# Kernel tuning notes

Hardware: AMD Instinct MI355X
Metric: run time of the kernel (lower is better)

The kernel has to match this reference:

```python
import jax, jax.numpy as jnp
import numpy as np

N, E, G = 100000, 800000, 1
DV, DE, DU, H = 64, 32, 32, 128

def _w(key, shape):
    return jax.random.normal(key, shape, dtype=jnp.float32) * 0.05

def setup_inputs() -> dict:
    key = jax.random.key(0)
    ks = jax.random.split(key, 16)
    inp = {
        "node_attr": jax.random.normal(ks[0], (N, DV), dtype=jnp.float32),
        "edges": jax.random.randint(ks[1], (2, E), 0, N, dtype=jnp.int64 if jax.config.jax_enable_x64 else jnp.int32),
        "edge_attr": jax.random.normal(ks[2], (E, DE), dtype=jnp.float32),
        "u": jax.random.normal(ks[3], (G, DU), dtype=jnp.float32),
        "node_idx": jnp.zeros((N,), dtype=jnp.int32),
        "edge_idx": jnp.zeros((E,), dtype=jnp.int32),
        # edge MLP: concat(src, dst, edge_attr, u) -> H -> H
        "W1e": _w(ks[4], (2 * DV + DE + DU, H)), "b1e": jnp.zeros((H,), jnp.float32),
        "W2e": _w(ks[5], (H, H)), "b2e": jnp.zeros((H,), jnp.float32),
        # node MLP: concat(node_attr, aggregated_edges, u) -> H -> H
        "W1n": _w(ks[6], (DV + H + DU, H)), "b1n": jnp.zeros((H,), jnp.float32),
        "W2n": _w(ks[7], (H, H)), "b2n": jnp.zeros((H,), jnp.float32),
        # global MLP: concat(node_mean, edge_mean, u) -> H -> H
        "W1g": _w(ks[8], (H + H + DU, H)), "b1g": jnp.zeros((H,), jnp.float32),
        "W2g": _w(ks[9], (H, H)), "b2g": jnp.zeros((H,), jnp.float32),
    }
    return inp

def _mlp(x, W1, b1, W2, b2):
    return jax.nn.relu(x @ W1 + b1) @ W2 + b2

def _seg_mean(x, seg, num):
    s = jax.ops.segment_sum(x, seg, num_segments=num)
    c = jax.ops.segment_sum(jnp.ones((x.shape[0], 1), x.dtype), seg, num_segments=num)
    return s / jnp.maximum(c, 1.0)

def reference(node_attr, edges, edge_attr, u, node_idx, edge_idx,
              W1e, b1e, W2e, b2e, W1n, b1n, W2n, b2n, W1g, b1g, W2g, b2g):
    row, col = edges[0], edges[1]
    # edge model: gather endpoint features, concat with edge/global attrs
    e_in = jnp.concatenate([node_attr[row], node_attr[col], edge_attr, u[edge_idx]], axis=-1)
    e = _mlp(e_in, W1e, b1e, W2e, b2e)                        # [E, H]
    # node model: scatter-add incoming edge messages onto receivers (col)
    agg = jax.ops.segment_sum(e, col, num_segments=node_attr.shape[0])  # [N, H]
    v_in = jnp.concatenate([node_attr, agg, u[node_idx]], axis=-1)
    v = _mlp(v_in, W1n, b1n, W2n, b2n)                        # [N, H]
    # global model: per-graph mean pooling of nodes and edges
    nv = _seg_mean(v, node_idx, u.shape[0])                   # [G, H]
    ne = _seg_mean(e, edge_idx, u.shape[0])                   # [G, H]
    g_in = jnp.concatenate([nv, ne, u], axis=-1)
    g = _mlp(g_in, W1g, b1g, W2g, b2g)                        # [G, H]
    return v, e, g
```

## Files before the change

kernel.cpp:

```cpp
#include <hip/hip_runtime.h>

#define N_NODES 100000
#define N_EDGES 800000
#define DV 64
#define DE 32
#define DU 32
#define H 128

#define NTILES 12500

typedef short bf16x8 __attribute__((ext_vector_type(8)));
typedef unsigned short u16;
typedef u16 u16x8 __attribute__((ext_vector_type(8)));
typedef float f32x4 __attribute__((ext_vector_type(4)));

#define OFF_ESUM 0
#define OFF_VSUM 8192
#define OFF_BIAS 16384
#define OFF_PART 17408
#define OFF_WBUF 19456
#define OFF_DEG  175104
#define OFF_SE   575104
#define OFF_DSTP 6975104

#define W1ET_OFF 0
#define W2ET_OFF 20480
#define W1NT_OFF 36864
#define W2NT_OFF 61440
#define WBUF_ELEMS 77824

#define NPART 391

__device__ inline u16 f2bf(float x) {
  union { float f; unsigned u; } c; c.f = x;
  unsigned r = c.u + 0x7FFFu + ((c.u >> 16) & 1u);
  return (u16)(r >> 16);
}

__global__ void prep_weights(const float* __restrict__ W1e, const float* __restrict__ W2e,
                             const float* __restrict__ W1n, const float* __restrict__ W2n,
                             u16* __restrict__ wbuf) {
  int i = blockIdx.x * blockDim.x + threadIdx.x;
  if (i < 20480) {
    int j = i / 160, k = i - j * 160;
    wbuf[W1ET_OFF + i] = f2bf(W1e[k * H + j]);
  } else if (i < 36864) {
    int t = i - 20480; int j = t >> 7, k = t & 127;
    wbuf[i] = f2bf(W2e[k * H + j]);
  } else if (i < 61440) {
    int t = i - 36864; int j = t / 192, k = t - j * 192;
    wbuf[i] = f2bf(W1n[k * H + j]);
  } else if (i < WBUF_ELEMS) {
    int t = i - 61440; int j = t >> 7, k = t & 127;
    wbuf[i] = f2bf(W2n[k * H + j]);
  }
}

__global__ void prep_bias(const float* __restrict__ uattr,
                          const float* __restrict__ W1e, const float* __restrict__ b1e,
                          const float* __restrict__ W1n, const float* __restrict__ b1n,
                          float* __restrict__ bias) {
  int t = threadIdx.x;
  float be = b1e[t];
  float bn = b1n[t];
  for (int k = 0; k < DU; ++k) {
    float uk = uattr[k];
    be += uk * W1e[(2 * DV + DE + k) * H + t];
    bn += uk * W1n[(DV + H + k) * H + t];
  }
  bias[t] = be;
  bias[128 + t] = bn;
}

__global__ void degree_kernel(const int* __restrict__ edges, int* __restrict__ deg) {
  int i = blockIdx.x * 256 + threadIdx.x;
  if (i < N_EDGES) atomicAdd(&deg[edges[N_EDGES + i]], 1);
}

__global__ void scan_part(const int* __restrict__ deg, int* __restrict__ part) {
  int i = blockIdx.x * 256 + threadIdx.x;
  int v = (i < N_NODES) ? deg[i] : 0;
#pragma unroll
  for (int m = 1; m < 64; m <<= 1) v += __shfl_xor(v, m);
  __shared__ int s[4];
  if ((threadIdx.x & 63) == 0) s[threadIdx.x >> 6] = v;
  __syncthreads();
  if (threadIdx.x == 0) part[blockIdx.x] = s[0] + s[1] + s[2] + s[3];
}

__global__ void scan_top(int* __restrict__ part) {
  __shared__ int s[512];
  int t = threadIdx.x;
  s[t] = (t < NPART) ? part[t] : 0;
  __syncthreads();
  for (int d = 1; d < 512; d <<= 1) {
    int v = (t >= d) ? s[t - d] : 0;
    __syncthreads();
    s[t] += v;
    __syncthreads();
  }
  if (t < NPART) part[t] = (t == 0) ? 0 : s[t - 1];
}

__global__ void scan_down(const int* __restrict__ part, int* __restrict__ deg_cursor) {
  __shared__ int s[256];
  int b = blockIdx.x, t = threadIdx.x;
  int i = b * 256 + t;
  int v = (i < N_NODES) ? deg_cursor[i] : 0;
  s[t] = v;
  __syncthreads();
  for (int d = 1; d < 256; d <<= 1) {
    int u = (t >= d) ? s[t - d] : 0;
    __syncthreads();
    s[t] += u;
    __syncthreads();
  }
  int excl = s[t] - v + part[b];
  if (i < N_NODES) deg_cursor[i] = excl;
}

__global__ void fill_kernel(const int* __restrict__ edges, int* __restrict__ cursor,
                            int2* __restrict__ se, int* __restrict__ dstP) {
  int i = blockIdx.x * 256 + threadIdx.x;
  if (i < N_EDGES) {
    int s = edges[i];
    int d = edges[N_EDGES + i];
    int pos = atomicAdd(&cursor[d], 1);
    se[pos] = make_int2(s, i);
    dstP[pos] = d;
  }
}

__global__ __launch_bounds__(256, 4) void edge_kernel(
    const float* __restrict__ node_attr, const float* __restrict__ edge_attr,
    const u16* __restrict__ wbuf, const float* __restrict__ bias_f,
    const float* __restrict__ b2,
    const int2* __restrict__ se, const int* __restrict__ dstP,
    float* __restrict__ e_out, float* __restrict__ agg, float* __restrict__ esum_p)
{
  __shared__ __align__(16) char smem[37888];
  u16 (*X)[164]    = (u16(*)[164])smem;
  u16 (*Hs)[132]   = (u16(*)[132])(smem + 20992);
  float (*OT)[132] = (float(*)[132])smem;
  __shared__ int sSrc[64], sEid[64], sDst[64];

  const int tid = threadIdx.x;
  const int wave = tid >> 6, lane = tid & 63;
  const int l15 = lane & 15, lg = lane >> 4;
  const int wc = wave * 32;

  int b = blockIdx.x;
  const int q = NTILES / 8, r8 = NTILES % 8;
  int xcd = b & 7, pos = b >> 3;
  long t = (xcd < r8 ? xcd * (q + 1) : r8 * (q + 1) + (xcd - r8) * q) + pos;
  const long i0 = t * 64;

  if (tid < 64)        { int2 v = se[i0 + tid]; sSrc[tid] = v.x; sEid[tid] = v.y; }
  else if (tid < 128)  sDst[tid - 64] = dstP[i0 + (tid - 64)];

  bf16x8 w1[5][2];
  {
    const u16* w1t = wbuf + W1ET_OFF;
#pragma unroll
    for (int cf = 0; cf < 2; ++cf) {
      const u16* p1 = w1t + (wc + cf * 16 + l15) * 160 + lg * 8;
#pragma unroll
      for (int ks = 0; ks < 5; ++ks) w1[ks][cf] = *(const bf16x8*)(p1 + ks * 32);
    }
  }
  float bias1[2] = { bias_f[wc + l15], bias_f[wc + 16 + l15] };

  __syncthreads();

#pragma unroll
  for (int it = 0; it < 5; ++it) {
    int ch = tid + it * 256;
    int r = ch / 20, g = ch - r * 20;
    int col = g * 8;
    const float* src;
    if (col < 64)        src = node_attr + (long)sSrc[r] * DV + col;
    else if (col < 128)  src = node_attr + (long)sDst[r] * DV + (col - 64);
    else                 src = edge_attr + (long)sEid[r] * DE + (col - 128);
    float4 f0 = *(const float4*)src;
    float4 f1 = *(const float4*)(src + 4);
    u16x8 p;
    p[0] = f2bf(f0.x); p[1] = f2bf(f0.y); p[2] = f2bf(f0.z); p[3] = f2bf(f0.w);
    p[4] = f2bf(f1.x); p[5] = f2bf(f1.y); p[6] = f2bf(f1.z); p[7] = f2bf(f1.w);
    *(u16x8*)&X[r][col] = p;
  }

  __syncthreads();

  f32x4 acc[4][2];
#pragma unroll
  for (int rf = 0; rf < 4; ++rf)
#pragma unroll
    for (int cf = 0; cf < 2; ++cf)
#pragma unroll
      for (int j = 0; j < 4; ++j) acc[rf][cf][j] = 0.f;

#pragma unroll
  for (int ks = 0; ks < 5; ++ks) {
#pragma unroll
    for (int rf = 0; rf < 4; ++rf) {
      bf16x8 a = *(const bf16x8*)&X[rf * 16 + l15][ks * 32 + lg * 8];
      acc[rf][0] = __builtin_amdgcn_mfma_f32_16x16x32_bf16(a, w1[ks][0], acc[rf][0], 0, 0, 0);
      acc[rf][1] = __builtin_amdgcn_mfma_f32_16x16x32_bf16(a, w1[ks][1], acc[rf][1], 0, 0, 0);
    }
  }

  bf16x8 w2[4][2];
  {
    const u16* w2t = wbuf + W2ET_OFF;
#pragma unroll
    for (int cf = 0; cf < 2; ++cf) {
      const u16* p2 = w2t + (wc + cf * 16 + l15) * 128 + lg * 8;
#pragma unroll
      for (int ks = 0; ks < 4; ++ks) w2[ks][cf] = *(const bf16x8*)(p2 + ks * 32);
    }
  }
  float bias2[2] = { b2[wc + l15], b2[wc + 16 + l15] };

#pragma unroll
  for (int rf = 0; rf < 4; ++rf)
#pragma unroll
    for (int cf = 0; cf < 2; ++cf)
#pragma unroll
      for (int j = 0; j < 4; ++j) {
        float hv = acc[rf][cf][j] + bias1[cf];
        hv = hv > 0.f ? hv : 0.f;
        Hs[rf * 16 + lg * 4 + j][wc + cf * 16 + l15] = f2bf(hv);
      }

  __syncthreads();

#pragma unroll
  for (int rf = 0; rf < 4; ++rf)
#pragma unroll
    for (int cf = 0; cf < 2; ++cf)
#pragma unroll
      for (int j = 0; j < 4; ++j) acc[rf][cf][j] = 0.f;

#pragma unroll
  for (int ks = 0; ks < 4; ++ks) {
#pragma unroll
    for (int rf = 0; rf < 4; ++rf) {
      bf16x8 a = *(const bf16x8*)&Hs[rf * 16 + l15][ks * 32 + lg * 8];
      acc[rf][0] = __builtin_amdgcn_mfma_f32_16x16x32_bf16(a, w2[ks][0], acc[rf][0], 0, 0, 0);
      acc[rf][1] = __builtin_amdgcn_mfma_f32_16x16x32_bf16(a, w2[ks][1], acc[rf][1], 0, 0, 0);
    }
  }

  __syncthreads();

  float es0 = 0.f, es1 = 0.f;
#pragma unroll
  for (int rf = 0; rf < 4; ++rf) {
#pragma unroll
    for (int cf = 0; cf < 2; ++cf) {
#pragma unroll
      for (int j = 0; j < 4; ++j) {
        float v = acc[rf][cf][j] + bias2[cf];
        OT[rf * 16 + lg * 4 + j][wc + cf * 16 + l15] = v;
        if (cf == 0) es0 += v; else es1 += v;
      }
    }
  }

  __syncthreads();

#pragma unroll
  for (int i = 0; i < 8; ++i) {
    int ch = tid + i * 256;
    int r = ch >> 5, c4 = ch & 31;
    float4 f = *(const float4*)&OT[r][c4 * 4];
    *(float4*)(e_out + (long)sEid[r] * H + c4 * 4) = f;
  }

  {
    const int c = tid & 127;
    const int rlo = (tid >> 7) * 32;
    float sum = 0.f;
    int runStart = rlo;
#pragma unroll 8
    for (int r = rlo; r < rlo + 32; ++r) {
      sum += OT[r][c];
      bool bnd = (r == rlo + 31) || (sDst[r + 1] != sDst[r]);
      if (bnd) {
        float* p = &agg[(long)sDst[r] * H + c];
        if (runStart == rlo || r == rlo + 31) atomicAdd(p, sum);
        else *p = sum;
        sum = 0.f; runStart = r + 1;
      }
    }
  }

#pragma unroll
  for (int m = 16; m < 64; m <<= 1) { es0 += __shfl_xor(es0, m); es1 += __shfl_xor(es1, m); }
  if (lane < 16) {
    atomicAdd(&esum_p[(wc + lane) * 16], es0);
    atomicAdd(&esum_p[(wc + 16 + lane) * 16], es1);
  }
}

__global__ __launch_bounds__(256, 3) void node_kernel(
    const float* __restrict__ node_attr, const u16* __restrict__ wbuf,
    const float* __restrict__ bias_f, const float* __restrict__ b2,
    float* __restrict__ vio, float* __restrict__ vsum_p)
{
  __shared__ __align__(16) u16 X[64][196];
  __shared__ __align__(16) u16 Hs[64][132];

  const int tid = threadIdx.x;
  const int wave = tid >> 6, lane = tid & 63;
  const int l15 = lane & 15, lg = lane >> 4;
  const long n0 = (long)blockIdx.x * 64;
  const int wc = wave * 32;

#pragma unroll
  for (int it = 0; it < 6; ++it) {
    int ch = tid + it * 256;
    int r = ch / 24, g = ch - r * 24;
    int col = g * 8;
    long n = n0 + r; if (n >= N_NODES) n = N_NODES - 1;
    const float* src;
    if (col < 64)  src = node_attr + n * DV + col;
    else           src = vio + n * H + (col - 64);
    float4 f0 = *(const float4*)src;
    float4 f1 = *(const float4*)(src + 4);
    u16x8 p;
    p[0] = f2bf(f0.x); p[1] = f2bf(f0.y); p[2] = f2bf(f0.z); p[3] = f2bf(f0.w);
    p[4] = f2bf(f1.x); p[5] = f2bf(f1.y); p[6] = f2bf(f1.z); p[7] = f2bf(f1.w);
    *(u16x8*)&X[r][col] = p;
  }

  bf16x8 w1[6][2], w2[4][2];
  {
    const u16* w1t = wbuf + W1NT_OFF;
    const u16* w2t = wbuf + W2NT_OFF;
#pragma unroll
    for (int cf = 0; cf < 2; ++cf) {
      const u16* p1 = w1t + (wc + cf * 16 + l15) * 192 + lg * 8;
#pragma unroll
      for (int ks = 0; ks < 6; ++ks) w1[ks][cf] = *(const bf16x8*)(p1 + ks * 32);
      const u16* p2 = w2t + (wc + cf * 16 + l15) * 128 + lg * 8;
#pragma unroll
      for (int ks = 0; ks < 4; ++ks) w2[ks][cf] = *(const bf16x8*)(p2 + ks * 32);
    }
  }

  __syncthreads();

  f32x4 acc[4][2];
#pragma unroll
  for (int rf = 0; rf < 4; ++rf)
#pragma unroll
    for (int cf = 0; cf < 2; ++cf)
#pragma unroll
      for (int j = 0; j < 4; ++j) acc[rf][cf][j] = 0.f;

#pragma unroll
  for (int ks = 0; ks < 6; ++ks) {
#pragma unroll
    for (int rf = 0; rf < 4; ++rf) {
      bf16x8 a = *(const bf16x8*)&X[rf * 16 + l15][ks * 32 + lg * 8];
      acc[rf][0] = __builtin_amdgcn_mfma_f32_16x16x32_bf16(a, w1[ks][0], acc[rf][0], 0, 0, 0);
      acc[rf][1] = __builtin_amdgcn_mfma_f32_16x16x32_bf16(a, w1[ks][1], acc[rf][1], 0, 0, 0);
    }
  }

  float bias1[2] = { bias_f[128 + wc + l15], bias_f[128 + wc + 16 + l15] };
#pragma unroll
  for (int rf = 0; rf < 4; ++rf)
#pragma unroll
    for (int cf = 0; cf < 2; ++cf)
#pragma unroll
      for (int j = 0; j < 4; ++j) {
        float hv = acc[rf][cf][j] + bias1[cf];
        hv = hv > 0.f ? hv : 0.f;
        Hs[rf * 16 + lg * 4 + j][wc + cf * 16 + l15] = f2bf(hv);
      }

  __syncthreads();

#pragma unroll
  for (int rf = 0; rf < 4; ++rf)
#pragma unroll
    for (int cf = 0; cf < 2; ++cf)
#pragma unroll
      for (int j = 0; j < 4; ++j) acc[rf][cf][j] = 0.f;

#pragma unroll
  for (int ks = 0; ks < 4; ++ks) {
#pragma unroll
    for (int rf = 0; rf < 4; ++rf) {
      bf16x8 a = *(const bf16x8*)&Hs[rf * 16 + l15][ks * 32 + lg * 8];
      acc[rf][0] = __builtin_amdgcn_mfma_f32_16x16x32_bf16(a, w2[ks][0], acc[rf][0], 0, 0, 0);
      acc[rf][1] = __builtin_amdgcn_mfma_f32_16x16x32_bf16(a, w2[ks][1], acc[rf][1], 0, 0, 0);
    }
  }

  float bias2[2] = { b2[wc + l15], b2[wc + 16 + l15] };
  float vs0 = 0.f, vs1 = 0.f;
#pragma unroll
  for (int rf = 0; rf < 4; ++rf) {
#pragma unroll
    for (int cf = 0; cf < 2; ++cf) {
      int colg = wc + cf * 16 + l15;
#pragma unroll
      for (int j = 0; j < 4; ++j) {
        int r = rf * 16 + lg * 4 + j;
        long n = n0 + r;
        if (n < N_NODES) {
          float v = acc[rf][cf][j] + bias2[cf];
          vio[n * H + colg] = v;
          if (cf == 0) vs0 += v; else vs1 += v;
        }
      }
    }
  }
#pragma unroll
  for (int m = 16; m < 64; m <<= 1) { vs0 += __shfl_xor(vs0, m); vs1 += __shfl_xor(vs1, m); }
  if (lane < 16) {
    atomicAdd(&vsum_p[(wc + lane) * 16], vs0);
    atomicAdd(&vsum_p[(wc + 16 + lane) * 16], vs1);
  }
}

__global__ void global_kernel(const float* __restrict__ uattr,
    const float* __restrict__ W1g, const float* __restrict__ b1g,
    const float* __restrict__ W2g, const float* __restrict__ b2g,
    const float* __restrict__ esum_p, const float* __restrict__ vsum_p,
    float* __restrict__ g_out)
{
  __shared__ float gin[288];
  __shared__ float hbuf[128];
  int t = threadIdx.x;
  gin[t]       = vsum_p[t * 16] * (1.f / (float)N_NODES);
  gin[128 + t] = esum_p[t * 16] * (1.f / (float)N_EDGES);
  if (t < 32) gin[256 + t] = uattr[t];
  __syncthreads();
  float a = b1g[t];
  for (int k = 0; k < 288; ++k) a += gin[k] * W1g[k * H + t];
  hbuf[t] = fmaxf(a, 0.f);
  __syncthreads();
  float b = b2g[t];
  for (int k = 0; k < 128; ++k) b += hbuf[k] * W2g[k * H + t];
  g_out[t] = b;
}

extern "C" void kernel_launch(void* const* d_in, const int* in_sizes, int n_in,
                              void* d_out, int out_size, void* d_ws, size_t ws_size,
                              hipStream_t stream) {
  const float* node_attr = (const float*)d_in[0];
  const int*   edges     = (const int*)d_in[1];
  const float* edge_attr = (const float*)d_in[2];
  const float* uattr     = (const float*)d_in[3];
  const float* W1e = (const float*)d_in[6];  const float* b1e = (const float*)d_in[7];
  const float* W2e = (const float*)d_in[8];  const float* b2e = (const float*)d_in[9];
  const float* W1n = (const float*)d_in[10]; const float* b1n = (const float*)d_in[11];
  const float* W2n = (const float*)d_in[12]; const float* b2n = (const float*)d_in[13];
  const float* W1g = (const float*)d_in[14]; const float* b1g = (const float*)d_in[15];
  const float* W2g = (const float*)d_in[16]; const float* b2g = (const float*)d_in[17];

  float* out   = (float*)d_out;
  float* v_out = out;
  float* e_out = out + (long)N_NODES * H;
  float* g_out = out + (long)N_NODES * H + (long)N_EDGES * H;

  char* ws = (char*)d_ws;
  float* esum_p = (float*)(ws + OFF_ESUM);
  float* vsum_p = (float*)(ws + OFF_VSUM);
  float* bias_f = (float*)(ws + OFF_BIAS);
  int*   part   = (int*)(ws + OFF_PART);
  u16*   wbuf   = (u16*)(ws + OFF_WBUF);
  int*   deg    = (int*)(ws + OFF_DEG);
  int2*  se     = (int2*)(ws + OFF_SE);
  int*   dstP   = (int*)(ws + OFF_DSTP);

  hipMemsetAsync(ws, 0, 16384, stream);
  hipMemsetAsync(deg, 0, N_NODES * sizeof(int), stream);
  hipMemsetAsync(v_out, 0, (size_t)N_NODES * H * sizeof(float), stream);

  prep_weights<<<WBUF_ELEMS / 256, 256, 0, stream>>>(W1e, W2e, W1n, W2n, wbuf);
  prep_bias<<<1, 128, 0, stream>>>(uattr, W1e, b1e, W1n, b1n, bias_f);
  degree_kernel<<<(N_EDGES + 255) / 256, 256, 0, stream>>>(edges, deg);
  scan_part<<<NPART, 256, 0, stream>>>(deg, part);
  scan_top<<<1, 512, 0, stream>>>(part);
  scan_down<<<NPART, 256, 0, stream>>>(part, deg);
  fill_kernel<<<(N_EDGES + 255) / 256, 256, 0, stream>>>(edges, deg, se, dstP);

  edge_kernel<<<NTILES, 256, 0, stream>>>(node_attr, edge_attr, wbuf,
                                          bias_f, b2e, se, dstP,
                                          e_out, v_out, esum_p);
  node_kernel<<<(N_NODES + 63) / 64, 256, 0, stream>>>(node_attr, wbuf,
                                                       bias_f, b2n, v_out, vsum_p);
  global_kernel<<<1, 128, 0, stream>>>(uattr, W1g, b1g, W2g, b2g, esum_p, vsum_p, g_out);
}
```

Baseline: 665.3 us.

## Replace atomic scatter aggregation with CSR gather in node kernel

The edge kernel now processes edges in their original order, so the edge_attr reads and e_out writes are contiguous, and it no longer scatters messages into agg with atomics. The node kernel instead walks a CSR bucket of incoming edge ids and sums their e_out rows to build the aggregate, which also removes the v_out memset. Both kernels move to 512-thread blocks with larger tiles. The cost is an extra random read of e_out (800K×128 floats) in the node kernel, and the row-run coalescing of atomics that the sorted layout gave is lost.

```diff
diff --git a/kernel.cpp b/kernel.cpp
--- a/kernel.cpp
+++ b/kernel.cpp
@@ -7,7 +7,8 @@
 #define DU 32
 #define H 128
 
-#define NTILES 12500
+#define ETILE 128
+#define NTILES_E (N_EDGES / ETILE)
 
 typedef short bf16x8 __attribute__((ext_vector_type(8)));
 typedef unsigned short u16;
@@ -20,8 +21,8 @@
 #define OFF_PART 17408
 #define OFF_WBUF 19456
 #define OFF_DEG  175104
-#define OFF_SE   575104
-#define OFF_DSTP 6975104
+#define OFF_OFFS 575104
+#define OFF_BUCK 975104
 
 #define W1ET_OFF 0
 #define W2ET_OFF 20480
@@ -102,7 +103,8 @@
   if (t < NPART) part[t] = (t == 0) ? 0 : s[t - 1];
 }
 
-__global__ void scan_down(const int* __restrict__ part, int* __restrict__ deg_cursor) {
+__global__ void scan_down(const int* __restrict__ part, int* __restrict__ deg_cursor,
+                          int* __restrict__ offsets) {
   __shared__ int s[256];
   int b = blockIdx.x, t = threadIdx.x;
   int i = b * 256 + t;
@@ -116,47 +118,41 @@
     __syncthreads();
   }
   int excl = s[t] - v + part[b];
-  if (i < N_NODES) deg_cursor[i] = excl;
+  if (i < N_NODES) { offsets[i] = excl; deg_cursor[i] = excl; }
 }
 
 __global__ void fill_kernel(const int* __restrict__ edges, int* __restrict__ cursor,
-                            int2* __restrict__ se, int* __restrict__ dstP) {
+                            int* __restrict__ bucket) {
   int i = blockIdx.x * 256 + threadIdx.x;
   if (i < N_EDGES) {
-    int s = edges[i];
     int d = edges[N_EDGES + i];
     int pos = atomicAdd(&cursor[d], 1);
-    se[pos] = make_int2(s, i);
-    dstP[pos] = d;
-  }
-}
-
-__global__ __launch_bounds__(256, 4) void edge_kernel(
-    const float* __restrict__ node_attr, const float* __restrict__ edge_attr,
+    bucket[pos] = i;
+  }
+}
+
+__global__ __launch_bounds__(512, 2) void edge_kernel(
+    const float* __restrict__ node_attr, const int* __restrict__ edges,
+    const float* __restrict__ edge_attr,
     const u16* __restrict__ wbuf, const float* __restrict__ bias_f,
     const float* __restrict__ b2,
-    const int2* __restrict__ se, const int* __restrict__ dstP,
-    float* __restrict__ e_out, float* __restrict__ agg, float* __restrict__ esum_p)
+    float* __restrict__ e_out, float* __restrict__ esum_p)
 {
-  __shared__ __align__(16) char smem[37888];
+  __shared__ __align__(16) char smem[75776];
   u16 (*X)[164]    = (u16(*)[164])smem;
-  u16 (*Hs)[132]   = (u16(*)[132])(smem + 20992);
+  u16 (*Hs)[132]   = (u16(*)[132])(smem + 41984);
   float (*OT)[132] = (float(*)[132])smem;
-  __shared__ int sSrc[64], sEid[64], sDst[64];
+  __shared__ int sSrc[128], sDst[128];
 
   const int tid = threadIdx.x;
   const int wave = tid >> 6, lane = tid & 63;
   const int l15 = lane & 15, lg = lane >> 4;
-  const int wc = wave * 32;
-
-  int b = blockIdx.x;
-  const int q = NTILES / 8, r8 = NTILES % 8;
-  int xcd = b & 7, pos = b >> 3;
-  long t = (xcd < r8 ? xcd * (q + 1) : r8 * (q + 1) + (xcd - r8) * q) + pos;
-  const long i0 = t * 64;
-
-  if (tid < 64)        { int2 v = se[i0 + tid]; sSrc[tid] = v.x; sEid[tid] = v.y; }
-  else if (tid < 128)  sDst[tid - 64] = dstP[i0 + (tid - 64)];
+  const int wc = (wave & 3) * 32;
+  const int rh = (wave >> 2) * 64;
+  const long e0 = (long)blockIdx.x * ETILE;
+
+  if (tid < 128)       sSrc[tid]       = edges[e0 + tid];
+  else if (tid < 256)  sDst[tid - 128] = edges[(long)N_EDGES + e0 + (tid - 128)];
 
   bf16x8 w1[5][2];
   {
@@ -172,15 +168,190 @@
 
   __syncthreads();
 
-#pragma unroll
-  for (int it = 0; it < 5; ++it) {
-    int ch = tid + it * 256;
-    int r = ch / 20, g = ch - r * 20;
-    int col = g * 8;
-    const float* src;
-    if (col < 64)        src = node_attr + (long)sSrc[r] * DV + col;
-    else if (col < 128)  src = node_attr + (long)sDst[r] * DV + (col - 64);
-    else                 src = edge_attr + (long)sEid[r] * DE + (col - 128);
+  {
+    float4 g0[5], g1[5];
+    int r_[5], c_[5];
+#pragma unroll
+    for (int it = 0; it < 5; ++it) {
+      int ch = tid + it * 512;
+      int r = ch / 20, gseg = ch - r * 20;
+      int col = gseg * 8;
+      r_[it] = r; c_[it] = col;
+      const float* src;
+      if (col < 64)        src = node_attr + (long)sSrc[r] * DV + col;
+      else if (col < 128)  src = node_attr + (long)sDst[r] * DV + (col - 64);
+      else                 src = edge_attr + (e0 + r) * DE + (col - 128);
+      g0[it] = *(const float4*)src;
+      g1[it] = *(const float4*)(src + 4);
+    }
+#pragma unroll
+    for (int it = 0; it < 5; ++it) {
+      u16x8 p;
+      p[0] = f2bf(g0[it].x); p[1] = f2bf(g0[it].y); p[2] = f2bf(g0[it].z); p[3] = f2bf(g0[it].w);
+      p[4] = f2bf(g1[it].x); p[5] = f2bf(g1[it].y); p[6] = f2bf(g1[it].z); p[7] = f2bf(g1[it].w);
+      *(u16x8*)&X[r_[it]][c_[it]] = p;
+    }
+  }
+
+  __syncthreads();
+
+  f32x4 acc[4][2];
+#pragma unroll
+  for (int rf = 0; rf < 4; ++rf)
+#pragma unroll
+    for (int cf = 0; cf < 2; ++cf)
+#pragma unroll
+      for (int j = 0; j < 4; ++j) acc[rf][cf][j] = 0.f;
+
+#pragma unroll
+  for (int ks = 0; ks < 5; ++ks) {
+#pragma unroll
+    for (int rf = 0; rf < 4; ++rf) {
+      bf16x8 a = *(const bf16x8*)&X[rh + rf * 16 + l15][ks * 32 + lg * 8];
+      acc[rf][0] = __builtin_amdgcn_mfma_f32_16x16x32_bf16(a, w1[ks][0], acc[rf][0], 0, 0, 0);
+      acc[rf][1] = __builtin_amdgcn_mfma_f32_16x16x32_bf16(a, w1[ks][1], acc[rf][1], 0, 0, 0);
+    }
+  }
+
+  bf16x8 w2[4][2];
+  {
+    const u16* w2t = wbuf + W2ET_OFF;
+#pragma unroll
+    for (int cf = 0; cf < 2; ++cf) {
+      const u16* p2 = w2t + (wc + cf * 16 + l15) * 128 + lg * 8;
+#pragma unroll
+      for (int ks = 0; ks < 4; ++ks) w2[ks][cf] = *(const bf16x8*)(p2 + ks * 32);
+    }
+  }
+  float bias2[2] = { b2[wc + l15], b2[wc + 16 + l15] };
+
+#pragma unroll
+  for (int rf = 0; rf < 4; ++rf)
+#pragma unroll
+    for (int cf = 0; cf < 2; ++cf)
+#pragma unroll
+      for (int j = 0; j < 4; ++j) {
+        float hv = acc[rf][cf][j] + bias1[cf];
+        hv = hv > 0.f ? hv : 0.f;
+        Hs[rh + rf * 16 + lg * 4 + j][wc + cf * 16 + l15] = f2bf(hv);
+      }
+
+  __syncthreads();
+
+#pragma unroll
+  for (int rf = 0; rf < 4; ++rf)
+#pragma unroll
+    for (int cf = 0; cf < 2; ++cf)
+#pragma unroll
+      for (int j = 0; j < 4; ++j) acc[rf][cf][j] = 0.f;
+
+#pragma unroll
+  for (int ks = 0; ks < 4; ++ks) {
+#pragma unroll
+    for (int rf = 0; rf < 4; ++rf) {
+      bf16x8 a = *(const bf16x8*)&Hs[rh + rf * 16 + l15][ks * 32 + lg * 8];
+      acc[rf][0] = __builtin_amdgcn_mfma_f32_16x16x32_bf16(a, w2[ks][0], acc[rf][0], 0, 0, 0);
+      acc[rf][1] = __builtin_amdgcn_mfma_f32_16x16x32_bf16(a, w2[ks][1], acc[rf][1], 0, 0, 0);
+    }
+  }
+
+  __syncthreads();
+
+  float es0 = 0.f, es1 = 0.f;
+#pragma unroll
+  for (int rf = 0; rf < 4; ++rf) {
+#pragma unroll
+    for (int cf = 0; cf < 2; ++cf) {
+#pragma unroll
+      for (int j = 0; j < 4; ++j) {
+        float v = acc[rf][cf][j] + bias2[cf];
+        OT[rh + rf * 16 + lg * 4 + j][wc + cf * 16 + l15] = v;
+        if (cf == 0) es0 += v; else es1 += v;
+      }
+    }
+  }
+
+  __syncthreads();
+
+#pragma unroll
+  for (int i = 0; i < 8; ++i) {
+    int ch = tid + i * 512;
+    int r = ch >> 5, c4 = ch & 31;
+    float4 f = *(const float4*)&OT[r][c4 * 4];
+    *(float4*)(e_out + (e0 + r) * H + c4 * 4) = f;
+  }
+
+#pragma unroll
+  for (int m = 16; m < 64; m <<= 1) { es0 += __shfl_xor(es0, m); es1 += __shfl_xor(es1, m); }
+  if (lane < 16) {
+    atomicAdd(&esum_p[(wc + lane) * 16], es0);
+    atomicAdd(&esum_p[(wc + 16 + lane) * 16], es1);
+  }
+}
+
+__global__ __launch_bounds__(512, 2) void node_kernel(
+    const float* __restrict__ node_attr, const u16* __restrict__ wbuf,
+    const float* __restrict__ bias_f, const float* __restrict__ b2,
+    const float* __restrict__ e_out, const int* __restrict__ offsets,
+    const int* __restrict__ cursor, const int* __restrict__ bucket,
+    float* __restrict__ v_out, float* __restrict__ vsum_p)
+{
+  __shared__ __align__(16) u16 X[64][196];
+  __shared__ __align__(16) u16 Hs[64][132];
+
+  const int tid = threadIdx.x;
+  const int wave = tid >> 6, lane = tid & 63;
+  const int l15 = lane & 15, lg = lane >> 4;
+  const int wc = (wave & 3) * 32;
+  const int rh = (wave >> 2) * 32;
+  const long n0 = (long)blockIdx.x * 64;
+
+  {
+    int gr = tid >> 3, gs = tid & 7;
+    long gn = n0 + gr; if (gn >= N_NODES) gn = N_NODES - 1;
+    float a[16];
+#pragma unroll
+    for (int k = 0; k < 16; ++k) a[k] = 0.f;
+    int s = offsets[gn], e = cursor[gn];
+    int i = s;
+    for (; i + 2 <= e; i += 2) {
+      const float* p0 = e_out + (long)bucket[i] * H + gs * 16;
+      const float* p1 = e_out + (long)bucket[i + 1] * H + gs * 16;
+      float4 f0[4], f1[4];
+#pragma unroll
+      for (int k = 0; k < 4; ++k) f0[k] = *(const float4*)(p0 + k * 4);
+#pragma unroll
+      for (int k = 0; k < 4; ++k) f1[k] = *(const float4*)(p1 + k * 4);
+#pragma unroll
+      for (int k = 0; k < 4; ++k) {
+        a[k * 4 + 0] += f0[k].x + f1[k].x;
+        a[k * 4 + 1] += f0[k].y + f1[k].y;
+        a[k * 4 + 2] += f0[k].z + f1[k].z;
+        a[k * 4 + 3] += f0[k].w + f1[k].w;
+      }
+    }
+    if (i < e) {
+      const float* p0 = e_out + (long)bucket[i] * H + gs * 16;
+#pragma unroll
+      for (int k = 0; k < 4; ++k) {
+        float4 f = *(const float4*)(p0 + k * 4);
+        a[k * 4 + 0] += f.x; a[k * 4 + 1] += f.y;
+        a[k * 4 + 2] += f.z; a[k * 4 + 3] += f.w;
+      }
+    }
+#pragma unroll
+    for (int k = 0; k < 2; ++k) {
+      u16x8 pk;
+#pragma unroll
+      for (int j = 0; j < 8; ++j) pk[j] = f2bf(a[k * 8 + j]);
+      *(u16x8*)&X[gr][64 + gs * 16 + k * 8] = pk;
+    }
+  }
+
+  {
+    int r = tid >> 3, col = (tid & 7) * 8;
+    long n = n0 + r; if (n >= N_NODES) n = N_NODES - 1;
+    const float* src = node_attr + n * DV + col;
     float4 f0 = *(const float4*)src;
     float4 f1 = *(const float4*)(src + 4);
     u16x8 p;
@@ -189,151 +360,6 @@
     *(u16x8*)&X[r][col] = p;
   }
 
-  __syncthreads();
-
-  f32x4 acc[4][2];
-#pragma unroll
-  for (int rf = 0; rf < 4; ++rf)
-#pragma unroll
-    for (int cf = 0; cf < 2; ++cf)
-#pragma unroll
-      for (int j = 0; j < 4; ++j) acc[rf][cf][j] = 0.f;
-
-#pragma unroll
-  for (int ks = 0; ks < 5; ++ks) {
-#pragma unroll
-    for (int rf = 0; rf < 4; ++rf) {
-      bf16x8 a = *(const bf16x8*)&X[rf * 16 + l15][ks * 32 + lg * 8];
-      acc[rf][0] = __builtin_amdgcn_mfma_f32_16x16x32_bf16(a, w1[ks][0], acc[rf][0], 0, 0, 0);
-      acc[rf][1] = __builtin_amdgcn_mfma_f32_16x16x32_bf16(a, w1[ks][1], acc[rf][1], 0, 0, 0);
-    }
-  }
-
-  bf16x8 w2[4][2];
-  {
-    const u16* w2t = wbuf + W2ET_OFF;
-#pragma unroll
-    for (int cf = 0; cf < 2; ++cf) {
-      const u16* p2 = w2t + (wc + cf * 16 + l15) * 128 + lg * 8;
-#pragma unroll
-      for (int ks = 0; ks < 4; ++ks) w2[ks][cf] = *(const bf16x8*)(p2 + ks * 32);
-    }
-  }
-  float bias2[2] = { b2[wc + l15], b2[wc + 16 + l15] };
-
-#pragma unroll
-  for (int rf = 0; rf < 4; ++rf)
-#pragma unroll
-    for (int cf = 0; cf < 2; ++cf)
-#pragma unroll
-      for (int j = 0; j < 4; ++j) {
-        float hv = acc[rf][cf][j] + bias1[cf];
-        hv = hv > 0.f ? hv : 0.f;
-        Hs[rf * 16 + lg * 4 + j][wc + cf * 16 + l15] = f2bf(hv);
-      }
-
-  __syncthreads();
-
-#pragma unroll
-  for (int rf = 0; rf < 4; ++rf)
-#pragma unroll
-    for (int cf = 0; cf < 2; ++cf)
-#pragma unroll
-      for (int j = 0; j < 4; ++j) acc[rf][cf][j] = 0.f;
-
-#pragma unroll
-  for (int ks = 0; ks < 4; ++ks) {
-#pragma unroll
-    for (int rf = 0; rf < 4; ++rf) {
-      bf16x8 a = *(const bf16x8*)&Hs[rf * 16 + l15][ks * 32 + lg * 8];
-      acc[rf][0] = __builtin_amdgcn_mfma_f32_16x16x32_bf16(a, w2[ks][0], acc[rf][0], 0, 0, 0);
-      acc[rf][1] = __builtin_amdgcn_mfma_f32_16x16x32_bf16(a, w2[ks][1], acc[rf][1], 0, 0, 0);
-    }
-  }
-
-  __syncthreads();
-
-  float es0 = 0.f, es1 = 0.f;
-#pragma unroll
-  for (int rf = 0; rf < 4; ++rf) {
-#pragma unroll
-    for (int cf = 0; cf < 2; ++cf) {
-#pragma unroll
-      for (int j = 0; j < 4; ++j) {
-        float v = acc[rf][cf][j] + bias2[cf];
-        OT[rf * 16 + lg * 4 + j][wc + cf * 16 + l15] = v;
-        if (cf == 0) es0 += v; else es1 += v;
-      }
-    }
-  }
-
-  __syncthreads();
-
-#pragma unroll
-  for (int i = 0; i < 8; ++i) {
-    int ch = tid + i * 256;
-    int r = ch >> 5, c4 = ch & 31;
-    float4 f = *(const float4*)&OT[r][c4 * 4];
-    *(float4*)(e_out + (long)sEid[r] * H + c4 * 4) = f;
-  }
-
-  {
-    const int c = tid & 127;
-    const int rlo = (tid >> 7) * 32;
-    float sum = 0.f;
-    int runStart = rlo;
-#pragma unroll 8
-    for (int r = rlo; r < rlo + 32; ++r) {
-      sum += OT[r][c];
-      bool bnd = (r == rlo + 31) || (sDst[r + 1] != sDst[r]);
-      if (bnd) {
-        float* p = &agg[(long)sDst[r] * H + c];
-        if (runStart == rlo || r == rlo + 31) atomicAdd(p, sum);
-        else *p = sum;
-        sum = 0.f; runStart = r + 1;
-      }
-    }
-  }
-
-#pragma unroll
-  for (int m = 16; m < 64; m <<= 1) { es0 += __shfl_xor(es0, m); es1 += __shfl_xor(es1, m); }
-  if (lane < 16) {
-    atomicAdd(&esum_p[(wc + lane) * 16], es0);
-    atomicAdd(&esum_p[(wc + 16 + lane) * 16], es1);
-  }
-}
-
-__global__ __launch_bounds__(256, 3) void node_kernel(
-    const float* __restrict__ node_attr, const u16* __restrict__ wbuf,
-    const float* __restrict__ bias_f, const float* __restrict__ b2,
-    float* __restrict__ vio, float* __restrict__ vsum_p)
-{
-  __shared__ __align__(16) u16 X[64][196];
-  __shared__ __align__(16) u16 Hs[64][132];
-
-  const int tid = threadIdx.x;
-  const int wave = tid >> 6, lane = tid & 63;
-  const int l15 = lane & 15, lg = lane >> 4;
-  const long n0 = (long)blockIdx.x * 64;
-  const int wc = wave * 32;
-
-#pragma unroll
-  for (int it = 0; it < 6; ++it) {
-    int ch = tid + it * 256;
-    int r = ch / 24, g = ch - r * 24;
-    int col = g * 8;
-    long n = n0 + r; if (n >= N_NODES) n = N_NODES - 1;
-    const float* src;
-    if (col < 64)  src = node_attr + n * DV + col;
-    else           src = vio + n * H + (col - 64);
-    float4 f0 = *(const float4*)src;
-    float4 f1 = *(const float4*)(src + 4);
-    u16x8 p;
-    p[0] = f2bf(f0.x); p[1] = f2bf(f0.y); p[2] = f2bf(f0.z); p[3] = f2bf(f0.w);
-    p[4] = f2bf(f1.x); p[5] = f2bf(f1.y); p[6] = f2bf(f1.z); p[7] = f2bf(f1.w);
-    *(u16x8*)&X[r][col] = p;
-  }
-
   bf16x8 w1[6][2], w2[4][2];
   {
     const u16* w1t = wbuf + W1NT_OFF;
@@ -351,9 +377,9 @@
 
   __syncthreads();
 
-  f32x4 acc[4][2];
-#pragma unroll
-  for (int rf = 0; rf < 4; ++rf)
+  f32x4 acc[2][2];
+#pragma unroll
+  for (int rf = 0; rf < 2; ++rf)
 #pragma unroll
     for (int cf = 0; cf < 2; ++cf)
 #pragma unroll
@@ -362,8 +388,8 @@
 #pragma unroll
   for (int ks = 0; ks < 6; ++ks) {
 #pragma unroll
-    for (int rf = 0; rf < 4; ++rf) {
-      bf16x8 a = *(const bf16x8*)&X[rf * 16 + l15][ks * 32 + lg * 8];
+    for (int rf = 0; rf < 2; ++rf) {
+      bf16x8 a = *(const bf16x8*)&X[rh + rf * 16 + l15][ks * 32 + lg * 8];
       acc[rf][0] = __builtin_amdgcn_mfma_f32_16x16x32_bf16(a, w1[ks][0], acc[rf][0], 0, 0, 0);
       acc[rf][1] = __builtin_amdgcn_mfma_f32_16x16x32_bf16(a, w1[ks][1], acc[rf][1], 0, 0, 0);
     }
@@ -371,20 +397,20 @@
 
   float bias1[2] = { bias_f[128 + wc + l15], bias_f[128 + wc + 16 + l15] };
 #pragma unroll
-  for (int rf = 0; rf < 4; ++rf)
+  for (int rf = 0; rf < 2; ++rf)
 #pragma unroll
     for (int cf = 0; cf < 2; ++cf)
 #pragma unroll
       for (int j = 0; j < 4; ++j) {
         float hv = acc[rf][cf][j] + bias1[cf];
         hv = hv > 0.f ? hv : 0.f;
-        Hs[rf * 16 + lg * 4 + j][wc + cf * 16 + l15] = f2bf(hv);
+        Hs[rh + rf * 16 + lg * 4 + j][wc + cf * 16 + l15] = f2bf(hv);
       }
 
   __syncthreads();
 
 #pragma unroll
-  for (int rf = 0; rf < 4; ++rf)
+  for (int rf = 0; rf < 2; ++rf)
 #pragma unroll
     for (int cf = 0; cf < 2; ++cf)
 #pragma unroll
@@ -393,8 +419,8 @@
 #pragma unroll
   for (int ks = 0; ks < 4; ++ks) {
 #pragma unroll
-    for (int rf = 0; rf < 4; ++rf) {
-      bf16x8 a = *(const bf16x8*)&Hs[rf * 16 + l15][ks * 32 + lg * 8];
+    for (int rf = 0; rf < 2; ++rf) {
+      bf16x8 a = *(const bf16x8*)&Hs[rh + rf * 16 + l15][ks * 32 + lg * 8];
       acc[rf][0] = __builtin_amdgcn_mfma_f32_16x16x32_bf16(a, w2[ks][0], acc[rf][0], 0, 0, 0);
       acc[rf][1] = __builtin_amdgcn_mfma_f32_16x16x32_bf16(a, w2[ks][1], acc[rf][1], 0, 0, 0);
     }
@@ -403,17 +429,17 @@
   float bias2[2] = { b2[wc + l15], b2[wc + 16 + l15] };
   float vs0 = 0.f, vs1 = 0.f;
 #pragma unroll
-  for (int rf = 0; rf < 4; ++rf) {
+  for (int rf = 0; rf < 2; ++rf) {
 #pragma unroll
     for (int cf = 0; cf < 2; ++cf) {
       int colg = wc + cf * 16 + l15;
 #pragma unroll
       for (int j = 0; j < 4; ++j) {
-        int r = rf * 16 + lg * 4 + j;
+        int r = rh + rf * 16 + lg * 4 + j;
         long n = n0 + r;
         if (n < N_NODES) {
           float v = acc[rf][cf][j] + bias2[cf];
-          vio[n * H + colg] = v;
+          v_out[n * H + colg] = v;
           if (cf == 0) vs0 += v; else vs1 += v;
         }
       }
@@ -475,25 +501,25 @@
   int*   part   = (int*)(ws + OFF_PART);
   u16*   wbuf   = (u16*)(ws + OFF_WBUF);
   int*   deg    = (int*)(ws + OFF_DEG);
-  int2*  se     = (int2*)(ws + OFF_SE);
-  int*   dstP   = (int*)(ws + OFF_DSTP);
+  int*   offs   = (int*)(ws + OFF_OFFS);
+  int*   buck   = (int*)(ws + OFF_BUCK);
 
   hipMemsetAsync(ws, 0, 16384, stream);
   hipMemsetAsync(deg, 0, N_NODES * sizeof(int), stream);
-  hipMemsetAsync(v_out, 0, (size_t)N_NODES * H * sizeof(float), stream);
 
   prep_weights<<<WBUF_ELEMS / 256, 256, 0, stream>>>(W1e, W2e, W1n, W2n, wbuf);
   prep_bias<<<1, 128, 0, stream>>>(uattr, W1e, b1e, W1n, b1n, bias_f);
   degree_kernel<<<(N_EDGES + 255) / 256, 256, 0, stream>>>(edges, deg);
   scan_part<<<NPART, 256, 0, stream>>>(deg, part);
   scan_top<<<1, 512, 0, stream>>>(part);
-  scan_down<<<NPART, 256, 0, stream>>>(part, deg);
-  fill_kernel<<<(N_EDGES + 255) / 256, 256, 0, stream>>>(edges, deg, se, dstP);
-
-  edge_kernel<<<NTILES, 256, 0, stream>>>(node_attr, edge_attr, wbuf,
-                                          bias_f, b2e, se, dstP,
-                                          e_out, v_out, esum_p);
-  node_kernel<<<(N_NODES + 63) / 64, 256, 0, stream>>>(node_attr, wbuf,
-                                                       bias_f, b2n, v_out, vsum_p);
+  scan_down<<<NPART, 256, 0, stream>>>(part, deg, offs);
+  fill_kernel<<<(N_EDGES + 255) / 256, 256, 0, stream>>>(edges, deg, buck);
+
+  edge_kernel<<<NTILES_E, 512, 0, stream>>>(node_attr, edges, edge_attr, wbuf,
+                                            bias_f, b2e, e_out, esum_p);
+  node_kernel<<<(N_NODES + 63) / 64, 512, 0, stream>>>(node_attr, wbuf,
+                                                       bias_f, b2n,
+                                                       e_out, offs, deg, buck,
+                                                       v_out, vsum_p);
   global_kernel<<<1, 128, 0, stream>>>(uattr, W1g, b1g, W2g, b2g, esum_p, vsum_p, g_out);
 }
```

Result: faster. 626.5 us (-5.8%).
